# Performance work log

Hardware: AMD Instinct MI355X
Metric: run time of the kernel (lower is better)

Reference implementation:

```python
import jax, jax.numpy as jnp
import numpy as np

N, T, J, NB = 2048, 81, 16, 15
D_ATT, HEADS, SEQ, D_LIN, NOISE = 48, 6, 31, 256, 45
BN_EPS, LN_EPS, SLOPE = 1e-5, 1e-6, 0.01

# Human3.6M 16-joint skeleton bone (parent, child) pairs
_BONES = [(0,1),(1,2),(2,3),(0,4),(4,5),(5,6),(0,7),(7,8),(8,9),(9,10),(8,11),(11,12),(12,13),(8,14),(14,15)]
BONES_P = np.array([p for p, c in _BONES])
BONES_C = np.array([c for p, c in _BONES])
_parent = {c: p for p, c in _BONES}
_bone_of = {c: i for i, (p, c) in enumerate(_BONES)}
_M = np.zeros((NB, J), np.float32)  # M[i,j]=1 iff bone i lies on root->joint j chain
for j in range(1, J):
    jj = j
    while jj != 0:
        _M[_bone_of[jj], j] = 1.0
        jj = _parent[jj]
M_BONE2POSE = jnp.asarray(_M)
FIXED_MASK = jnp.ones((NB,), jnp.float32).at[jnp.array([6, 7])].set(0.0)  # torso bones kept fixed


def _layer_norm(t, a, b):
    mean = t.mean(-1, keepdims=True)
    # torch.std default is unbiased (ddof=1); module divides by (std + eps)
    std = jnp.sqrt(((t - mean) ** 2).sum(-1, keepdims=True) / (t.shape[-1] - 1))
    return a * (t - mean) / (std + LN_EPS) + b


def _leaky(x):
    return jnp.where(x >= 0, x, SLOPE * x)


def _axis_angle_to_matrix(v):
    # Rodrigues: v (..., 3) axis-angle -> (..., 3, 3)
    theta = jnp.linalg.norm(v, axis=-1, keepdims=True)
    k = v / jnp.maximum(theta, 1e-8)
    c = jnp.cos(theta)[..., None]
    s = jnp.sin(theta)[..., None]
    kx, ky, kz = k[..., 0], k[..., 1], k[..., 2]
    z = jnp.zeros_like(kx)
    K = jnp.stack([jnp.stack([z, -kz, ky], -1),
                   jnp.stack([kz, z, -kx], -1),
                   jnp.stack([-ky, kx, z], -1)], -2)
    kk = k[..., :, None] * k[..., None, :]
    return c * jnp.eye(3, dtype=v.dtype) + s * K + (1 - c) * kk


def setup_inputs() -> dict:
    key = jax.random.key(0)
    ks = jax.random.split(key, 12)
    w = lambda k, shape, scale=0.05: jax.random.normal(k, shape, jnp.float32) * scale
    return {
        'inputs_3d': jax.random.normal(ks[0], (N, 1, T, J, 3), jnp.float32),
        'noise': jax.random.normal(ks[1], (N, NOISE), jnp.float32),
        'enc_w': w(ks[2], (D_ATT, 3)), 'enc_b': jnp.zeros((D_ATT,), jnp.float32),
        'enc_bn_g': jnp.ones((D_ATT,), jnp.float32), 'enc_bn_b': jnp.zeros((D_ATT,), jnp.float32),
        'ln_a': jnp.ones((D_ATT,), jnp.float32), 'ln_b': jnp.zeros((D_ATT,), jnp.float32),
        'wq': w(ks[3], (D_ATT, D_ATT)), 'bq': jnp.zeros((D_ATT,), jnp.float32),
        'wk': w(ks[4], (D_ATT, D_ATT)), 'bk': jnp.zeros((D_ATT,), jnp.float32),
        'wv': w(ks[5], (D_ATT, D_ATT)), 'bv': jnp.zeros((D_ATT,), jnp.float32),
        'wo': w(ks[6], (D_ATT, D_ATT)), 'bo': jnp.zeros((D_ATT,), jnp.float32),
        'w1': w(ks[7], (D_LIN, SEQ * D_ATT)), 'b1': jnp.zeros((D_LIN,), jnp.float32),
        'bn1_g': jnp.ones((D_LIN,), jnp.float32), 'bn1_b': jnp.zeros((D_LIN,), jnp.float32),
        'w2': w(ks[8], (NB * 4, D_LIN)), 'b2': w(ks[9], (NB * 4,), 0.1),
    }


def reference(inputs_3d, noise, enc_w, enc_b, enc_bn_g, enc_bn_b, ln_a, ln_b,
              wq, bq, wk, bk, wv, bv, wo, bo, w1, b1, bn1_g, bn1_b, w2, b2):
    x5 = inputs_3d[:, 0]                                  # (n, T, 16, 3)
    root = x5[:, :, :1, :]
    x = x5 - root                                         # root-centered
    bvec = x[..., BONES_C, :] - x[..., BONES_P, :]        # (n, T, 15, 3)
    blen = jnp.linalg.norm(bvec, axis=-1, keepdims=True)
    bunit = bvec / blen
    n, t_len = x.shape[0], x.shape[1]
    mid = (t_len - 1) // 2

    x_ = x[:, mid].reshape(n, -1)                         # (n, 48)
    y = jnp.concatenate([x_, noise], axis=-1).reshape(n, SEQ, 3)
    # Conv1d(k=1) == per-token linear; BatchNorm eval (running mean 0, var 1); Dropout off
    y = jax.nn.relu((y @ enc_w.T + enc_b) * enc_bn_g / jnp.sqrt(1.0 + BN_EPS) + enc_bn_b)

    # tiny 6-head self-attention with pre-LayerNorm and residual
    h = _layer_norm(y, ln_a, ln_b)
    d = D_ATT // HEADS
    q = (h @ wq.T + bq).reshape(n, SEQ, HEADS, d).transpose(0, 2, 1, 3)
    k = (h @ wk.T + bk).reshape(n, SEQ, HEADS, d).transpose(0, 2, 1, 3)
    v = (h @ wv.T + bv).reshape(n, SEQ, HEADS, d).transpose(0, 2, 1, 3)
    probs = jax.nn.softmax(jnp.einsum('nhqd,nhkd->nhqk', q, k) / (d ** 0.5), axis=-1)
    ctx = jnp.einsum('nhqk,nhkd->nhqd', probs, v).transpose(0, 2, 1, 3).reshape(n, SEQ, D_ATT)
    y = y + (ctx @ wo.T + bo)

    y = y.reshape(n, -1)                                  # (n, 1488)
    y = _leaky((y @ w1.T + b1) * bn1_g / jnp.sqrt(1.0 + BN_EPS) + bn1_b)
    y = _leaky(y @ w2.T + b2).reshape(n, NB, 4)           # (n, 15, 4)

    axis = y[..., :3]
    axis = axis / jnp.linalg.norm(axis, axis=-1, keepdims=True)
    theta = y[..., 3:4] / t_len                           # (n, 15, 1)
    t_idx = jnp.arange(t_len, dtype=y.dtype)              # (T,)
    vaa = axis[:, None] * (theta[:, None] * t_idx[None, :, None, None])  # (n, T, 15, 3)
    R = _axis_angle_to_matrix(vaa)                        # (n, T, 15, 3, 3)
    mod_unit = jnp.einsum('ntbij,ntbj->ntbi', R, bunit)
    mask = FIXED_MASK[None, None, :, None]
    mod_unit = mod_unit * mask + bunit * (1 - mask)
    ba_diff = 1 - jnp.sum(mod_unit * bunit, axis=-1)      # (n, T, 15)
    mod_bone = mod_unit * blen
    out = jnp.einsum('ntbc,bj->ntjc', mod_bone, M_BONE2POSE) + root  # (n, T, 16, 3)
    return out, ba_diff
```

## Files before the change

### kernel.cpp

```cpp
#include <hip/hip_runtime.h>
#include <math.h>

#define NS   2048
#define TL   81
#define NBN  15
#define DA   48
#define SQL  31
#define KD   1488
#define DL   256
#define MID  40

#define INV_SQRT_BN 0.99999500003749969f
#define SCALE_ATT   0.35355339059327373f

__global__ __launch_bounds__(256)
void attn_kernel(const float* __restrict__ x5, const float* __restrict__ noise,
                 const float* __restrict__ enc_w, const float* __restrict__ enc_b,
                 const float* __restrict__ enc_g, const float* __restrict__ enc_bb,
                 const float* __restrict__ ln_a, const float* __restrict__ ln_b,
                 const float* __restrict__ wq, const float* __restrict__ bq,
                 const float* __restrict__ wk, const float* __restrict__ bk,
                 const float* __restrict__ wv, const float* __restrict__ bv,
                 const float* __restrict__ wo, const float* __restrict__ bo,
                 float* __restrict__ y2)
{
    __shared__ float s93[96];
    __shared__ float sy[32*49];
    __shared__ float sh[32*49];
    __shared__ float sW[3*48*49];
    __shared__ __align__(16) float sQKV[32*148];
    __shared__ float smean[32], sinv[32];

    const int tid = threadIdx.x;
    const int n = blockIdx.x;

    if (tid < 93) {
        float v;
        if (tid < 48) {
            const float* base = x5 + ((size_t)n*TL + MID)*48;
            v = base[tid] - base[tid % 3];
        } else {
            v = noise[(size_t)n*45 + (tid-48)];
        }
        s93[tid] = v;
    }
    #pragma unroll
    for (int l=0; l<9; l++){
        int idx = tid + l*256;
        int f = idx/48, c = idx - f*48;
        int o = f*49 + c;
        sW[o]        = wq[idx];
        sW[2352 + o] = wk[idx];
        sW[4704 + o] = wv[idx];
    }
    __syncthreads();

    for (int idx=tid; idx<SQL*DA; idx+=256){
        int s = idx/48, f = idx - s*48;
        float a = enc_b[f]
                + s93[s*3+0]*enc_w[f*3+0]
                + s93[s*3+1]*enc_w[f*3+1]
                + s93[s*3+2]*enc_w[f*3+2];
        float v = a * (enc_g[f]*INV_SQRT_BN) + enc_bb[f];
        sy[s*49+f] = fmaxf(v, 0.0f);
    }
    __syncthreads();

    if (tid < SQL){
        float m = 0.f;
        for (int f=0; f<48; f++) m += sy[tid*49+f];
        m *= (1.0f/48.0f);
        float vs = 0.f;
        for (int f=0; f<48; f++){ float d = sy[tid*49+f]-m; vs += d*d; }
        float sd = sqrtf(vs * (1.0f/47.0f));
        smean[tid] = m;
        sinv[tid]  = 1.0f/(sd + 1e-6f);
    }
    __syncthreads();

    for (int idx=tid; idx<SQL*DA; idx+=256){
        int s = idx/48, f = idx - s*48;
        sh[s*49+f] = ln_a[f]*(sy[s*49+f]-smean[s])*sinv[s] + ln_b[f];
    }
    __syncthreads();

    if (tid < 192){
        const int sg = tid/24, fg = tid - (tid/24)*24;
        const int arr = fg >> 3;
        const int f0  = (fg & 7)*6;
        const float* wb = sW + arr*2352 + f0*49;
        const float* hb = sh + sg*4*49;
        float a0[6]={0,0,0,0,0,0}, a1[6]={0,0,0,0,0,0};
        float a2[6]={0,0,0,0,0,0}, a3[6]={0,0,0,0,0,0};
        for (int c=0; c<48; c++){
            float h0 = hb[c], h1 = hb[49+c], h2 = hb[98+c], h3 = hb[147+c];
            #pragma unroll
            for (int i=0;i<6;i++){
                float w = wb[i*49+c];
                a0[i] += h0*w; a1[i] += h1*w; a2[i] += h2*w; a3[i] += h3*w;
            }
        }
        const float* bias = (arr==0)? bq : (arr==1? bk : bv);
        #pragma unroll
        for (int i=0;i<6;i++){
            float b = bias[f0+i];
            int col = arr*48 + f0 + i;
            sQKV[(sg*4+0)*148 + col] = a0[i] + b;
            sQKV[(sg*4+1)*148 + col] = a1[i] + b;
            sQKV[(sg*4+2)*148 + col] = a2[i] + b;
            sQKV[(sg*4+3)*148 + col] = a3[i] + b;
        }
    }
    __syncthreads();

    #pragma unroll
    for (int l=0; l<9; l++){
        int idx = tid + l*256;
        sW[(idx/48)*49 + (idx%48)] = wo[idx];
    }
    if (tid < 186){
        const int hd = tid/31, qi = tid - (tid/31)*31;
        const float4 q0 = *(const float4*)(sQKV + qi*148 + hd*8);
        const float4 q1 = *(const float4*)(sQKV + qi*148 + hd*8 + 4);
        float sc[31]; float mx = -1e30f;
        for (int ki=0; ki<31; ki++){
            const float4 k0 = *(const float4*)(sQKV + ki*148 + 48 + hd*8);
            const float4 k1 = *(const float4*)(sQKV + ki*148 + 48 + hd*8 + 4);
            float d = q0.x*k0.x + q0.y*k0.y + q0.z*k0.z + q0.w*k0.w
                    + q1.x*k1.x + q1.y*k1.y + q1.z*k1.z + q1.w*k1.w;
            d *= SCALE_ATT;
            sc[ki] = d; mx = fmaxf(mx, d);
        }
        float ssum = 0.f;
        for (int ki=0; ki<31; ki++){ float e = expf(sc[ki]-mx); sc[ki]=e; ssum += e; }
        float rin = 1.0f/ssum;
        float4 c0 = {0,0,0,0}, c1 = {0,0,0,0};
        for (int ki=0; ki<31; ki++){
            float p = sc[ki];
            const float4 v0 = *(const float4*)(sQKV + ki*148 + 96 + hd*8);
            const float4 v1 = *(const float4*)(sQKV + ki*148 + 96 + hd*8 + 4);
            c0.x += p*v0.x; c0.y += p*v0.y; c0.z += p*v0.z; c0.w += p*v0.w;
            c1.x += p*v1.x; c1.y += p*v1.y; c1.z += p*v1.z; c1.w += p*v1.w;
        }
        float* cb = sh + qi*49 + hd*8;
        cb[0]=c0.x*rin; cb[1]=c0.y*rin; cb[2]=c0.z*rin; cb[3]=c0.w*rin;
        cb[4]=c1.x*rin; cb[5]=c1.y*rin; cb[6]=c1.z*rin; cb[7]=c1.w*rin;
    }
    __syncthreads();

    if (tid < 192){
        const int sg = tid/12, fg = tid - (tid/12)*12;
        const int f0 = fg*4;
        const float* wb = sW + f0*49;
        const float* cb = sh + sg*2*49;
        float a0[4]={0,0,0,0}, a1[4]={0,0,0,0};
        for (int c=0; c<48; c++){
            float x0 = cb[c], x1 = cb[49+c];
            #pragma unroll
            for (int i=0;i<4;i++){
                float w = wb[i*49+c];
                a0[i] += x0*w; a1[i] += x1*w;
            }
        }
        {
            int s = sg*2;
            if (s < 31){
                float* dst = y2 + (size_t)n*KD + s*48 + f0;
                const float* yb = sy + s*49 + f0;
                #pragma unroll
                for (int i=0;i<4;i++) dst[i] = yb[i] + a0[i] + bo[f0+i];
            }
        }
        {
            int s = sg*2+1;
            if (s < 31){
                float* dst = y2 + (size_t)n*KD + s*48 + f0;
                const float* yb = sy + s*49 + f0;
                #pragma unroll
                for (int i=0;i<4;i++) dst[i] = yb[i] + a1[i] + bo[f0+i];
            }
        }
    }
}

__global__ __launch_bounds__(256)
void gemm1_kernel(const float* __restrict__ y2, const float* __restrict__ w1,
                  const float* __restrict__ b1, const float* __restrict__ g1,
                  const float* __restrict__ bb1, float* __restrict__ y3)
{
    __shared__ __align__(16) float sA[48*20];
    __shared__ float sB[48*64];
    const int tid = threadIdx.x;
    const int bx = blockIdx.x;
    const int m0 = (bx >> 2) * 16;
    const int n0 = (bx & 3) * 64;
    const int c  = tid & 63;
    const int r0 = (tid >> 6) * 4;
    float acc0=0.f, acc1=0.f, acc2=0.f, acc3=0.f;

    for (int it=0; it<31; ++it){
        const int k0 = it*48;
        if (tid < 192){
            int r = tid/12, kb = (tid%12)*4;
            float4 v = *(const float4*)(y2 + (size_t)(m0+r)*KD + k0 + kb);
            sA[(kb+0)*20+r]=v.x; sA[(kb+1)*20+r]=v.y; sA[(kb+2)*20+r]=v.z; sA[(kb+3)*20+r]=v.w;
        }
        #pragma unroll
        for (int l=0;l<3;l++){
            int idx = tid + l*256;
            int cc = idx/12, kb = (idx%12)*4;
            float4 v = *(const float4*)(w1 + (size_t)(n0+cc)*KD + k0 + kb);
            sB[(kb+0)*64+cc]=v.x; sB[(kb+1)*64+cc]=v.y; sB[(kb+2)*64+cc]=v.z; sB[(kb+3)*64+cc]=v.w;
        }
        __syncthreads();
        #pragma unroll
        for (int kk=0; kk<48; kk++){
            float b = sB[kk*64 + c];
            float4 a = *(const float4*)(sA + kk*20 + r0);
            acc0 += a.x*b; acc1 += a.y*b; acc2 += a.z*b; acc3 += a.w*b;
        }
        __syncthreads();
    }
    const int col = n0 + c;
    const float scl = g1[col]*INV_SQRT_BN;
    const float sft = bb1[col];
    const float bs  = b1[col];
    float v0 = (acc0+bs)*scl+sft; v0 = v0>=0.f? v0 : 0.01f*v0;
    float v1 = (acc1+bs)*scl+sft; v1 = v1>=0.f? v1 : 0.01f*v1;
    float v2 = (acc2+bs)*scl+sft; v2 = v2>=0.f? v2 : 0.01f*v2;
    float v3 = (acc3+bs)*scl+sft; v3 = v3>=0.f? v3 : 0.01f*v3;
    const int m = m0 + r0;
    y3[(size_t)(m+0)*DL + col] = v0;
    y3[(size_t)(m+1)*DL + col] = v1;
    y3[(size_t)(m+2)*DL + col] = v2;
    y3[(size_t)(m+3)*DL + col] = v3;
}

__global__ __launch_bounds__(256)
void head_kernel(const float* __restrict__ y3, const float* __restrict__ w2,
                 const float* __restrict__ b2, float* __restrict__ at)
{
    __shared__ float swc[64*60];
    __shared__ __align__(16) float sy3[16*256];
    __shared__ float sy4[16*61];
    const int tid = threadIdx.x;
    const int n0 = blockIdx.x * 16;

    #pragma unroll
    for (int l=0;l<4;l++){
        int idx = tid + l*256;
        int s = idx >> 6, i4 = (idx & 63) << 2;
        *(float4*)(sy3 + s*256 + i4) = *(const float4*)(y3 + (size_t)(n0+s)*256 + i4);
    }

    float acc[4]; int ss[4], mm[4];
    #pragma unroll
    for (int l=0;l<4;l++){
        int uu = tid + l*256;
        ss[l]=0; mm[l]=0; acc[l]=0.f;
        if (uu < 960){ ss[l]=uu/60; mm[l]=uu-ss[l]*60; acc[l]=b2[mm[l]]; }
    }

    for (int ch=0; ch<4; ch++){
        const int i0 = ch*64;
        __syncthreads();
        #pragma unroll
        for (int l=0;l<15;l++){
            int idx = tid + l*256;
            int m = idx >> 6, io = idx & 63;
            swc[io*60 + m] = w2[(size_t)m*256 + i0 + io];
        }
        __syncthreads();
        #pragma unroll
        for (int l=0;l<4;l++){
            int uu = tid + l*256;
            if (uu < 960){
                const float* yy = sy3 + ss[l]*256 + i0;
                float a = acc[l];
                #pragma unroll 8
                for (int io=0; io<64; io++) a += yy[io]*swc[io*60 + mm[l]];
                acc[l] = a;
            }
        }
    }
    __syncthreads();
    #pragma unroll
    for (int l=0;l<4;l++){
        int uu = tid + l*256;
        if (uu < 960){
            float a = acc[l];
            sy4[ss[l]*61 + mm[l]] = a>=0.f? a : 0.01f*a;
        }
    }
    __syncthreads();
    if (tid < 240){
        int s = tid/15, b = tid - s*15;
        const float* y4 = sy4 + s*61 + b*4;
        float ax=y4[0], ay=y4[1], az=y4[2], th=y4[3];
        float nr = sqrtf(ax*ax+ay*ay+az*az);
        float4 o;
        o.x = ax/nr; o.y = ay/nr; o.z = az/nr; o.w = th/81.0f;
        *(float4*)(at + (size_t)(n0+s)*60 + b*4) = o;
    }
}

__global__ __launch_bounds__(256)
void pose_kernel(const float* __restrict__ x5, const float* __restrict__ at,
                 float* __restrict__ out)
{
    const int gid = blockIdx.x*256 + threadIdx.x;
    if (gid >= NS*TL) return;
    const int n = gid / TL;
    const int t = gid - n*TL;
    const float ft = (float)t;

    float4 pv[12];
    {
        const float4* src = (const float4*)(x5 + (size_t)gid*48);
        #pragma unroll
        for (int i=0;i<12;i++) pv[i] = src[i];
    }
    float* p = (float*)pv;
    const float4* ab = (const float4*)(at + (size_t)n*60);

    float4 posv[12];
    float* pos = (float*)posv;
    pos[0]=p[0]; pos[1]=p[1]; pos[2]=p[2];
    float ba[15];

    const int PJ[15] = {0,1,2,0,4,5,0,7,8,9,8,11,12,8,14};
    const int CJ[15] = {1,2,3,4,5,6,7,8,9,10,11,12,13,14,15};

    #pragma unroll
    for (int b=0;b<15;b++){
        const int pj = PJ[b], cj = CJ[b];
        float bx = p[cj*3+0]-p[pj*3+0];
        float by = p[cj*3+1]-p[pj*3+1];
        float bz = p[cj*3+2]-p[pj*3+2];
        float bl = sqrtf(bx*bx+by*by+bz*bz);
        float ux = bx/bl, uy = by/bl, uz = bz/bl;
        float mx, my, mz;
        if (b==6 || b==7){
            mx=ux; my=uy; mz=uz;
        } else {
            float4 a = ab[b];
            float ang = a.w * ft;
            float cs = cosf(ang), sn = sinf(ang);
            float kd = a.x*ux + a.y*uy + a.z*uz;
            float cx = a.y*uz - a.z*uy;
            float cy = a.z*ux - a.x*uz;
            float cz = a.x*uy - a.y*ux;
            float oc = (1.0f-cs)*kd;
            mx = ux*cs + cx*sn + a.x*oc;
            my = uy*cs + cy*sn + a.y*oc;
            mz = uz*cs + cz*sn + a.z*oc;
        }
        ba[b] = 1.0f - (mx*ux+my*uy+mz*uz);
        pos[cj*3+0] = pos[pj*3+0] + mx*bl;
        pos[cj*3+1] = pos[pj*3+1] + my*bl;
        pos[cj*3+2] = pos[pj*3+2] + mz*bl;
    }

    {
        float4* dst = (float4*)(out + (size_t)gid*48);
        #pragma unroll
        for (int i=0;i<12;i++) dst[i] = posv[i];
    }
    {
        float* bd = out + (size_t)NS*TL*48 + (size_t)gid*15;
        #pragma unroll
        for (int b=0;b<15;b++) bd[b] = ba[b];
    }
}

extern "C" void kernel_launch(void* const* d_in, const int* in_sizes, int n_in,
                              void* d_out, int out_size, void* d_ws, size_t ws_size,
                              hipStream_t stream)
{
    const float* x5    = (const float*)d_in[0];
    const float* noise = (const float*)d_in[1];
    const float* enc_w = (const float*)d_in[2];
    const float* enc_b = (const float*)d_in[3];
    const float* enc_g = (const float*)d_in[4];
    const float* enc_bb= (const float*)d_in[5];
    const float* ln_a  = (const float*)d_in[6];
    const float* ln_b  = (const float*)d_in[7];
    const float* wq = (const float*)d_in[8];
    const float* bq = (const float*)d_in[9];
    const float* wk = (const float*)d_in[10];
    const float* bk = (const float*)d_in[11];
    const float* wv = (const float*)d_in[12];
    const float* bv = (const float*)d_in[13];
    const float* wo = (const float*)d_in[14];
    const float* bo = (const float*)d_in[15];
    const float* w1 = (const float*)d_in[16];
    const float* b1 = (const float*)d_in[17];
    const float* g1 = (const float*)d_in[18];
    const float* bb1= (const float*)d_in[19];
    const float* w2 = (const float*)d_in[20];
    const float* b2 = (const float*)d_in[21];
    float* out = (float*)d_out;

    float* ws = (float*)d_ws;
    float* y2 = ws;
    float* y3 = y2 + (size_t)NS*KD;
    float* at = y3 + (size_t)NS*DL;

    attn_kernel<<<NS, 256, 0, stream>>>(x5, noise, enc_w, enc_b, enc_g, enc_bb,
                                        ln_a, ln_b, wq,bq,wk,bk,wv,bv,wo,bo, y2);
    gemm1_kernel<<<512, 256, 0, stream>>>(y2, w1, b1, g1, bb1, y3);
    head_kernel<<<128, 256, 0, stream>>>(y3, w2, b2, at);
    pose_kernel<<<(NS*TL+255)/256, 256, 0, stream>>>(x5, at, out);

    (void)in_sizes; (void)n_in; (void)out_size; (void)ws_size;
}
```

Baseline: 294.3 us.

## Split-K gemm1 with full-width N tiles and reduce partials in head kernel

```diff
diff --git a/kernel.cpp b/kernel.cpp
--- a/kernel.cpp
+++ b/kernel.cpp
@@ -183,62 +183,83 @@
     }
 }
 
+#define KSP 6
+#define KPS 248
+#define KCH 8
+
 __global__ __launch_bounds__(256)
 void gemm1_kernel(const float* __restrict__ y2, const float* __restrict__ w1,
-                  const float* __restrict__ b1, const float* __restrict__ g1,
-                  const float* __restrict__ bb1, float* __restrict__ y3)
+                  float* __restrict__ y3raw, int use_partial)
 {
-    __shared__ __align__(16) float sA[48*20];
-    __shared__ float sB[48*64];
+    __shared__ __align__(16) float sB[KCH*256];
+    __shared__ __align__(16) float sA[KCH*20];
     const int tid = threadIdx.x;
     const int bx = blockIdx.x;
-    const int m0 = (bx >> 2) * 16;
-    const int n0 = (bx & 3) * 64;
-    const int c  = tid & 63;
-    const int r0 = (tid >> 6) * 4;
-    float acc0=0.f, acc1=0.f, acc2=0.f, acc3=0.f;
-
-    for (int it=0; it<31; ++it){
-        const int k0 = it*48;
-        if (tid < 192){
-            int r = tid/12, kb = (tid%12)*4;
-            float4 v = *(const float4*)(y2 + (size_t)(m0+r)*KD + k0 + kb);
-            sA[(kb+0)*20+r]=v.x; sA[(kb+1)*20+r]=v.y; sA[(kb+2)*20+r]=v.z; sA[(kb+3)*20+r]=v.w;
-        }
-        #pragma unroll
-        for (int l=0;l<3;l++){
-            int idx = tid + l*256;
-            int cc = idx/12, kb = (idx%12)*4;
-            float4 v = *(const float4*)(w1 + (size_t)(n0+cc)*KD + k0 + kb);
-            sB[(kb+0)*64+cc]=v.x; sB[(kb+1)*64+cc]=v.y; sB[(kb+2)*64+cc]=v.z; sB[(kb+3)*64+cc]=v.w;
-        }
+    const int m0 = (bx & 127) * 16;
+    const int split = bx >> 7;
+    const int ks0 = split * KPS;
+    const int c0 = (tid & 15)*4 + (tid >> 6)*64;
+    const int r0 = ((tid >> 4) & 3)*4;
+
+    const int bn = tid >> 1;
+    const int bg = (tid & 1)*4;
+    const int ar = tid >> 1;
+    const int ag = (tid & 1)*4;
+
+    float acc[4][4];
+    #pragma unroll
+    for (int i=0;i<4;i++)
+        #pragma unroll
+        for (int j=0;j<4;j++) acc[i][j]=0.f;
+
+    for (int ch=0; ch<31; ch++){
+        const int k0 = ks0 + ch*KCH;
+        float4 b0v = *(const float4*)(w1 + (size_t)bn*KD        + k0 + bg);
+        float4 b1v = *(const float4*)(w1 + (size_t)(bn+128)*KD  + k0 + bg);
+        float4 av;
+        if (tid < 32) av = *(const float4*)(y2 + (size_t)(m0+ar)*KD + k0 + ag);
         __syncthreads();
-        #pragma unroll
-        for (int kk=0; kk<48; kk++){
-            float b = sB[kk*64 + c];
+        sB[(bg+0)*256 + bn] = b0v.x;  sB[(bg+1)*256 + bn] = b0v.y;
+        sB[(bg+2)*256 + bn] = b0v.z;  sB[(bg+3)*256 + bn] = b0v.w;
+        sB[(bg+0)*256 + bn+128] = b1v.x;  sB[(bg+1)*256 + bn+128] = b1v.y;
+        sB[(bg+2)*256 + bn+128] = b1v.z;  sB[(bg+3)*256 + bn+128] = b1v.w;
+        if (tid < 32){
+            sA[(ag+0)*20 + ar] = av.x;  sA[(ag+1)*20 + ar] = av.y;
+            sA[(ag+2)*20 + ar] = av.z;  sA[(ag+3)*20 + ar] = av.w;
+        }
+        __syncthreads();
+        #pragma unroll
+        for (int kk=0; kk<KCH; kk++){
+            float4 b = *(const float4*)(sB + kk*256 + c0);
             float4 a = *(const float4*)(sA + kk*20 + r0);
-            acc0 += a.x*b; acc1 += a.y*b; acc2 += a.z*b; acc3 += a.w*b;
-        }
-        __syncthreads();
-    }
-    const int col = n0 + c;
-    const float scl = g1[col]*INV_SQRT_BN;
-    const float sft = bb1[col];
-    const float bs  = b1[col];
-    float v0 = (acc0+bs)*scl+sft; v0 = v0>=0.f? v0 : 0.01f*v0;
-    float v1 = (acc1+bs)*scl+sft; v1 = v1>=0.f? v1 : 0.01f*v1;
-    float v2 = (acc2+bs)*scl+sft; v2 = v2>=0.f? v2 : 0.01f*v2;
-    float v3 = (acc3+bs)*scl+sft; v3 = v3>=0.f? v3 : 0.01f*v3;
-    const int m = m0 + r0;
-    y3[(size_t)(m+0)*DL + col] = v0;
-    y3[(size_t)(m+1)*DL + col] = v1;
-    y3[(size_t)(m+2)*DL + col] = v2;
-    y3[(size_t)(m+3)*DL + col] = v3;
+            acc[0][0] += a.x*b.x; acc[0][1] += a.x*b.y; acc[0][2] += a.x*b.z; acc[0][3] += a.x*b.w;
+            acc[1][0] += a.y*b.x; acc[1][1] += a.y*b.y; acc[1][2] += a.y*b.z; acc[1][3] += a.y*b.w;
+            acc[2][0] += a.z*b.x; acc[2][1] += a.z*b.y; acc[2][2] += a.z*b.z; acc[2][3] += a.z*b.w;
+            acc[3][0] += a.w*b.x; acc[3][1] += a.w*b.y; acc[3][2] += a.w*b.z; acc[3][3] += a.w*b.w;
+        }
+    }
+
+    if (use_partial){
+        float* dst = y3raw + (size_t)split*NS*DL;
+        #pragma unroll
+        for (int i=0;i<4;i++){
+            float4 v; v.x=acc[i][0]; v.y=acc[i][1]; v.z=acc[i][2]; v.w=acc[i][3];
+            *(float4*)(dst + (size_t)(m0+r0+i)*DL + c0) = v;
+        }
+    } else {
+        #pragma unroll
+        for (int i=0;i<4;i++)
+            #pragma unroll
+            for (int j=0;j<4;j++)
+                atomicAdd(y3raw + (size_t)(m0+r0+i)*DL + c0 + j, acc[i][j]);
+    }
 }
 
 __global__ __launch_bounds__(256)
-void head_kernel(const float* __restrict__ y3, const float* __restrict__ w2,
-                 const float* __restrict__ b2, float* __restrict__ at)
+void head_kernel(const float* __restrict__ y3raw, const float* __restrict__ w2,
+                 const float* __restrict__ b2, const float* __restrict__ b1,
+                 const float* __restrict__ g1, const float* __restrict__ bb1,
+                 float* __restrict__ at, int nsl)
 {
     __shared__ float swc[64*60];
     __shared__ __align__(16) float sy3[16*256];
@@ -250,7 +271,23 @@
     for (int l=0;l<4;l++){
         int idx = tid + l*256;
         int s = idx >> 6, i4 = (idx & 63) << 2;
-        *(float4*)(sy3 + s*256 + i4) = *(const float4*)(y3 + (size_t)(n0+s)*256 + i4);
+        const float* src = y3raw + (size_t)(n0+s)*256 + i4;
+        float4 v = *(const float4*)(src);
+        if (nsl == 6){
+            #pragma unroll
+            for (int sl=1; sl<6; sl++){
+                float4 p = *(const float4*)(src + (size_t)sl*NS*DL);
+                v.x += p.x; v.y += p.y; v.z += p.z; v.w += p.w;
+            }
+        }
+        const float4 vb = *(const float4*)(b1 + i4);
+        const float4 vg = *(const float4*)(g1 + i4);
+        const float4 vs = *(const float4*)(bb1 + i4);
+        v.x = (v.x + vb.x)*(vg.x*INV_SQRT_BN) + vs.x;  v.x = v.x>=0.f? v.x : 0.01f*v.x;
+        v.y = (v.y + vb.y)*(vg.y*INV_SQRT_BN) + vs.y;  v.y = v.y>=0.f? v.y : 0.01f*v.y;
+        v.z = (v.z + vb.z)*(vg.z*INV_SQRT_BN) + vs.z;  v.z = v.z>=0.f? v.z : 0.01f*v.z;
+        v.w = (v.w + vb.w)*(vg.w*INV_SQRT_BN) + vs.w;  v.w = v.w>=0.f? v.w : 0.01f*v.w;
+        *(float4*)(sy3 + s*256 + i4) = v;
     }
 
     float acc[4]; int ss[4], mm[4];
@@ -404,13 +441,20 @@
     float* ws = (float*)d_ws;
     float* y2 = ws;
     float* y3 = y2 + (size_t)NS*KD;
-    float* at = y3 + (size_t)NS*DL;
+
+    const size_t need_partial = ((size_t)NS*KD + 6*(size_t)NS*DL + (size_t)NS*60) * 4;
+    const int use_partial = (ws_size >= need_partial) ? 1 : 0;
+    const int nsl = use_partial ? 6 : 1;
+    float* at = y3 + (size_t)nsl*NS*DL;
+
+    if (!use_partial)
+        hipMemsetAsync(y3, 0, (size_t)NS*DL*sizeof(float), stream);
 
     attn_kernel<<<NS, 256, 0, stream>>>(x5, noise, enc_w, enc_b, enc_g, enc_bb,
                                         ln_a, ln_b, wq,bq,wk,bk,wv,bv,wo,bo, y2);
-    gemm1_kernel<<<512, 256, 0, stream>>>(y2, w1, b1, g1, bb1, y3);
-    head_kernel<<<128, 256, 0, stream>>>(y3, w2, b2, at);
+    gemm1_kernel<<<128*KSP, 256, 0, stream>>>(y2, w1, y3, use_partial);
+    head_kernel<<<128, 256, 0, stream>>>(y3, w2, b2, b1, g1, bb1, at, nsl);
     pose_kernel<<<(NS*TL+255)/256, 256, 0, stream>>>(x5, at, out);
 
-    (void)in_sizes; (void)n_in; (void)out_size; (void)ws_size;
+    (void)in_sizes; (void)n_in; (void)out_size;
 }
```

New measurement: 252.2 us. 1.17x faster.
